# Kernel tuning notes

Measured on AMD Instinct MI355X. Metric: run time of the kernel, lower is better.

Reference implementation:

```python
import math
import jax, jax.numpy as jnp
import numpy as np

# dims (from init_kwargs / forward signature)
B, N, K = 8, 1024, 8            # batch, nodes, num_neighbors
NC, TED, TEC = 64, 128, 64      # num_channels, time_embedding_dim, time_embedding_channels
C = NC + TEC                    # model dim = 128
H, Dh = 8, 16                   # heads, dim_head
HD = H * Dh
L = 4                           # num_layers
RH = 32                         # radial-net hidden width
NPATH = 10                      # radial scalars: k00,k10,k01,k11a,k11b,v00,v10,v01,v11a,v11b


def _g(k, shape, fan_in):
    return jax.random.normal(k, shape, dtype=jnp.float32) / np.sqrt(float(fan_in))


def setup_inputs() -> dict:
    key = jax.random.key(0)
    ks = jax.random.split(key, 16)
    return dict(
        x=jax.random.normal(ks[0], (B, N, 3), dtype=jnp.float32),
        y=jax.random.normal(ks[1], (B, N, 3), dtype=jnp.float32),
        t=jax.random.uniform(ks[2], (B,), dtype=jnp.float32) * 1000.0,
        Wt1=_g(ks[3], (TED, TED), TED), bt1=jnp.zeros((TED,), jnp.float32),
        Wt2=_g(ks[4], (TED, TEC), TED), bt2=jnp.zeros((TEC,), jnp.float32),
        Win0=_g(ks[5], (TEC + 3, C), TEC + 3), bin0=jnp.zeros((C,), jnp.float32),
        Win1=_g(ks[6], (1, C), 1),
        Wqkv=_g(ks[7], (L, 12, C, HD), C),           # q0,q1,k00,k10,k01,k11a,k11b,v00,v10,v01,v11a,v11b
        Wr1=_g(ks[8], (L, 1, RH), 1), br1=jnp.zeros((L, RH), jnp.float32),
        Wr2=_g(ks[9], (L, RH, H * NPATH), RH), br2=jnp.zeros((L, H * NPATH), jnp.float32),
        Wo=_g(ks[10], (L, 2, HD, C), HD), bo=jnp.zeros((L, 2, C), jnp.float32),
        Wout=_g(ks[11], (3, C), C), bout=jnp.zeros((3,), jnp.float32),
    )


def _forward(x, y, t, Wt1, bt1, Wt2, bt2, Win0, bin0, Win1, Wqkv,
             Wr1, br1, Wr2, br2, Wo, bo, Wout, bout):
    b, n = x.shape[0], x.shape[1]
    # sinusoidal time embedding + time MLP
    half = TED // 2
    freqs = jnp.exp(-math.log(10000.0) * jnp.arange(half, dtype=x.dtype) / half)
    emb = t[:, None] * freqs
    temb = jnp.concatenate([jnp.sin(emb), jnp.cos(emb)], axis=-1)          # [B,TED]
    temb = jax.nn.silu(temb @ Wt1 + bt1) @ Wt2 + bt2                        # [B,TEC]

    # degree-0 input = [time_embed | coords], degree-1 input = coords (1 channel)
    deg0 = jnp.concatenate([jnp.broadcast_to(temb[:, None, :], (b, n, TEC)), x], axis=-1)
    f0 = deg0 @ Win0 + bin0                                                 # [B,N,C]
    f1 = jnp.einsum('bnv,c->bncv', x, Win1[0])                              # [B,N,C,3]

    # k-nearest-neighbor graph on coordinates (shared across layers)
    d2 = jnp.sum((x[:, :, None, :] - x[:, None, :, :]) ** 2, axis=-1)       # [B,N,N]
    d2 = d2 + jnp.eye(n, dtype=x.dtype) * 1e9                               # exclude self
    _, idx = jax.lax.top_k(-d2, K)                                          # [B,N,K]
    gather = lambda f: jax.vmap(lambda a, i: a[i])(f, idx)                  # [B,N,...] -> [B,N,K,...]
    rel = gather(x) - x[:, :, None, :]                                      # [B,N,K,3]
    r = jnp.sqrt(jnp.sum(rel ** 2, axis=-1, keepdims=True) + 1e-8)          # [B,N,K,1]
    rhat = rel / r

    inv_scale = 1.0 / float(np.sqrt(2 * Dh))
    for l in range(L):
        Wl = Wqkv[l].reshape(12, C, H, Dh)
        q0 = jnp.einsum('bnc,chd->bnhd', f0, Wl[0])
        q1 = jnp.einsum('bncv,chd->bnhdv', f1, Wl[1])
        f0j, f1j = gather(f0), gather(f1)                                   # [B,N,K,C], [B,N,K,C,3]
        # radial network -> per-head, per-path scalars
        Rn = (jax.nn.silu(r @ Wr1[l] + br1[l]) @ Wr2[l] + br2[l]).reshape(b, n, K, H, NPATH)
        # equivariant tensor-product paths (degrees 0/1, spherical harmonics Y0,Y1,Y2)
        dot1 = jnp.einsum('bnkcv,bnkv->bnkc', f1j, rhat)                    # 1->0 path
        sym = 3.0 * dot1[..., None] * rhat[:, :, :, None, :] - f1j          # Y2 (traceless sym) 1->1 path
        p0 = lambda f, w: jnp.einsum('bnkc,chd->bnkhd', f, w)
        p1 = lambda f, w: jnp.einsum('bnkcv,chd->bnkhdv', f, w)
        rh = rhat[:, :, :, None, None, :]
        k0 = p0(f0j, Wl[2]) * Rn[..., 0:1] + p0(dot1, Wl[3]) * Rn[..., 1:2]
        k1 = (p0(f0j, Wl[4])[..., None] * rh * Rn[..., 2][..., None, None]
              + p1(f1j, Wl[5]) * Rn[..., 3][..., None, None]
              + p1(sym, Wl[6]) * Rn[..., 4][..., None, None])
        v0 = p0(f0j, Wl[7]) * Rn[..., 5:6] + p0(dot1, Wl[8]) * Rn[..., 6:7]
        v1 = (p0(f0j, Wl[9])[..., None] * rh * Rn[..., 7][..., None, None]
              + p1(f1j, Wl[10]) * Rn[..., 8][..., None, None]
              + p1(sym, Wl[11]) * Rn[..., 9][..., None, None])
        logits = (jnp.einsum('bnhd,bnkhd->bnhk', q0, k0)
                  + jnp.einsum('bnhdv,bnkhdv->bnhk', q1, k1)) * inv_scale
        attn = jax.nn.softmax(logits, axis=-1)
        o0 = jnp.einsum('bnhk,bnkhd->bnhd', attn, v0).reshape(b, n, HD)
        o1 = jnp.einsum('bnhk,bnkhdv->bnhdv', attn, v1).reshape(b, n, HD, 3)
        f0 = f0 + o0 @ Wo[l, 0] + bo[l, 0]
        f1 = f1 + jnp.einsum('bnev,ec->bncv', o1, Wo[l, 1]) + bo[l, 1][None, None, :, None]

    # output layer Linear(dim, 3) applied as per-component channel mixing on the type-1 output
    return jnp.einsum('bncv,vc->bnv', f1, Wout) + bout                      # [B,N,3]


def reference(x, y, t, Wt1, bt1, Wt2, bt2, Win0, bin0, Win1, Wqkv,
              Wr1, br1, Wr2, br2, Wo, bo, Wout, bout):
    return _forward(x, y, t, Wt1, bt1, Wt2, bt2, Win0, bin0, Win1, Wqkv,
                    Wr1, br1, Wr2, br2, Wo, bo, Wout, bout)
```

## Files before the change

kernel.cpp:

```cpp
#include <hip/hip_runtime.h>
#include <math.h>

#define NBATCH 8
#define NPTS   1024
#define KNN    8
#define CC     128
#define HD_    128
#define TED_   128
#define TEC_   64
#define RH     32
#define NL     4

typedef _Float16 half8 __attribute__((ext_vector_type(8)));
typedef _Float16 h2v  __attribute__((ext_vector_type(2)));
typedef float f32x4 __attribute__((ext_vector_type(4)));

__global__ __launch_bounds__(128) void k_temb(
    const float* __restrict__ t, const float* __restrict__ Wt1,
    const float* __restrict__ bt1, const float* __restrict__ Wt2,
    const float* __restrict__ bt2, const float* __restrict__ Win0,
    const float* __restrict__ bin0, float* __restrict__ pre0)
{
  int b = blockIdx.x;
  int tid = threadIdx.x;
  __shared__ float e128[TED_];
  __shared__ float h1[TED_];
  __shared__ float te[TEC_];
  float tv = t[b];
  if (tid < 64) {
    float fr = expf((-9.210340371976184f * (float)tid) * 0.015625f);
    float em = tv * fr;
    e128[tid]      = sinf(em);
    e128[tid + 64] = cosf(em);
  }
  __syncthreads();
  {
    float acc = bt1[tid];
    for (int i = 0; i < TED_; ++i) acc += e128[i] * Wt1[i * TED_ + tid];
    h1[tid] = acc / (1.0f + expf(-acc));
  }
  __syncthreads();
  if (tid < TEC_) {
    float acc = bt2[tid];
    for (int j = 0; j < TED_; ++j) acc += h1[j] * Wt2[j * TEC_ + tid];
    te[tid] = acc;
  }
  __syncthreads();
  {
    float acc = bin0[tid];
    for (int i = 0; i < TEC_; ++i) acc += te[i] * Win0[i * CC + tid];
    pre0[b * CC + tid] = acc;
  }
}

__global__ __launch_bounds__(256) void k_init(
    const float* __restrict__ x, const float* __restrict__ Win0,
    const float* __restrict__ Win1, const float* __restrict__ pre0,
    float* __restrict__ f0, float* __restrict__ f1,
    _Float16* __restrict__ f0h, _Float16* __restrict__ f1h)
{
  int node = blockIdx.x * 2 + (threadIdx.x >> 7);
  int c = threadIdx.x & 127;
  int b = node >> 10;
  float x0 = x[node * 3 + 0], x1 = x[node * 3 + 1], x2 = x[node * 3 + 2];
  float acc = pre0[b * CC + c]
            + x0 * Win0[(TEC_ + 0) * CC + c]
            + x1 * Win0[(TEC_ + 1) * CC + c]
            + x2 * Win0[(TEC_ + 2) * CC + c];
  f0[(size_t)node * CC + c] = acc;
  f0h[(size_t)node * CC + c] = (_Float16)acc;
  float w1 = Win1[c];
  float v0 = x0 * w1, v1 = x1 * w1, v2 = x2 * w1;
  f1[((size_t)node * 3 + 0) * CC + c] = v0;
  f1[((size_t)node * 3 + 1) * CC + c] = v1;
  f1[((size_t)node * 3 + 2) * CC + c] = v2;
  f1h[((size_t)node * 3 + 0) * CC + c] = (_Float16)v0;
  f1h[((size_t)node * 3 + 1) * CC + c] = (_Float16)v1;
  f1h[((size_t)node * 3 + 2) * CC + c] = (_Float16)v2;
}

__global__ __launch_bounds__(256) void k_knn(
    const float* __restrict__ x, int* __restrict__ idx,
    float* __restrict__ rhat, float* __restrict__ rl)
{
  const int b    = blockIdx.x >> 5;
  const int tile = blockIdx.x & 31;
  const int tid  = threadIdx.x;
  const int qg   = tid >> 3;
  const int sub  = tid & 7;

  __shared__ float xs[NPTS * 3];
  __shared__ unsigned long long keys[32][64];

  for (int i = tid; i < NPTS * 3; i += 256) xs[i] = x[(size_t)b * NPTS * 3 + i];
  __syncthreads();

  const int n = tile * 32 + qg;
  const float qx = xs[n * 3 + 0], qy = xs[n * 3 + 1], qz = xs[n * 3 + 2];

  unsigned long long bd[KNN];
  #pragma unroll
  for (int k = 0; k < KNN; ++k) bd[k] = ~0ull;

  const int j0 = sub * 128;
  for (int j = j0; j < j0 + 128; ++j) {
    float dx = qx - xs[j * 3 + 0];
    float dy = qy - xs[j * 3 + 1];
    float dz = qz - xs[j * 3 + 2];
    float s = __fadd_rn(__fadd_rn(__fmul_rn(dx, dx), __fmul_rn(dy, dy)),
                        __fmul_rn(dz, dz));
    if (j == n) s = 1.0e9f;
    unsigned long long key =
        ((unsigned long long)__float_as_uint(s) << 32) | (unsigned int)j;
    if (key < bd[KNN - 1]) {
      bd[KNN - 1] = key;
      #pragma unroll
      for (int q = KNN - 1; q > 0; --q) {
        if (bd[q] < bd[q - 1]) {
          unsigned long long tmp = bd[q]; bd[q] = bd[q - 1]; bd[q - 1] = tmp;
        }
      }
    }
  }
  #pragma unroll
  for (int k = 0; k < KNN; ++k) keys[qg][sub * KNN + k] = bd[k];
  __syncthreads();

  if (sub == 0) {
    unsigned long long m[KNN];
    #pragma unroll
    for (int k = 0; k < KNN; ++k) m[k] = ~0ull;
    for (int i = 0; i < 64; ++i) {
      unsigned long long key = keys[qg][i];
      if (key < m[KNN - 1]) {
        m[KNN - 1] = key;
        #pragma unroll
        for (int q = KNN - 1; q > 0; --q) {
          if (m[q] < m[q - 1]) {
            unsigned long long tmp = m[q]; m[q] = m[q - 1]; m[q - 1] = tmp;
          }
        }
      }
    }
    size_t base = ((size_t)b * NPTS + n) * KNN;
    #pragma unroll
    for (int k = 0; k < KNN; ++k) {
      int j = (int)(m[k] & 0xffffffffu);
      idx[base + k] = j;
      float rx = xs[j * 3 + 0] - qx;
      float ry = xs[j * 3 + 1] - qy;
      float rz = xs[j * 3 + 2] - qz;
      float rr2 = rx * rx + ry * ry + rz * rz + 1e-8f;
      float r = sqrtf(rr2);
      rl[base + k] = r;
      rhat[(base + k) * 3 + 0] = rx / r;
      rhat[(base + k) * 3 + 1] = ry / r;
      rhat[(base + k) * 3 + 2] = rz / r;
    }
  }
}

__global__ __launch_bounds__(256) void k_wconv(
    const float* __restrict__ Wqkv, const float* __restrict__ Wo,
    _Float16* __restrict__ Whq, _Float16* __restrict__ Who)
{
  __shared__ _Float16 T[128][136];
  int m = blockIdx.x;
  const float* src; _Float16* dst;
  if (m < 48) { src = Wqkv + (size_t)m * 16384; dst = Whq + (size_t)m * 16384; }
  else { src = Wo + (size_t)(m - 48) * 16384; dst = Who + (size_t)(m - 48) * 16384; }
  int tid = threadIdx.x;
  for (int i = tid; i < 16384; i += 256) {
    int k = i >> 7, n = i & 127;
    T[n][k] = (_Float16)src[i];
  }
  __syncthreads();
  for (int i = tid; i < 16384; i += 256) {
    int n = i >> 7, k = i & 127;
    dst[i] = T[n][k];
  }
}

#define MFMA_BODY(A_, ROWBASE_, WT_)                                          \
  const int tid  = threadIdx.x;                                               \
  const int lane = tid & 63;                                                  \
  const int w    = tid >> 6;                                                  \
  const int r15  = lane & 15;                                                 \
  const int g    = lane >> 4;                                                 \
  half8 bf[2][4];                                                             \
  _Pragma("unroll")                                                           \
  for (int ntl = 0; ntl < 2; ++ntl) {                                         \
    int n = (w * 2 + ntl) * 16 + r15;                                         \
    const _Float16* wp = (WT_) + (size_t)n * 128 + g * 8;                     \
    _Pragma("unroll")                                                         \
    for (int ks = 0; ks < 4; ++ks)                                            \
      bf[ntl][ks] = *(const half8*)(wp + ks * 32);                            \
  }                                                                           \
  {                                                                           \
    int r = tid >> 1;                                                         \
    const _Float16* src = (A_) + (size_t)((ROWBASE_) + r) * 128;              \
    int c0 = (tid & 1) * 8;                                                   \
    _Pragma("unroll")                                                         \
    for (int q = 0; q < 8; ++q) {                                             \
      int c = c0 + q;                                                         \
      *(uint4*)&As[r][c * 8] = *(const uint4*)(src + c * 8);                  \
    }                                                                         \
  }                                                                           \
  __syncthreads();                                                            \
  f32x4 acc[8][2] = {};                                                       \
  _Pragma("unroll")                                                           \
  for (int ks = 0; ks < 4; ++ks) {                                            \
    half8 a[8];                                                               \
    _Pragma("unroll")                                                         \
    for (int mt = 0; mt < 8; ++mt)                                            \
      a[mt] = *(const half8*)&As[mt * 16 + r15][ks * 32 + g * 8];             \
    _Pragma("unroll")                                                         \
    for (int mt = 0; mt < 8; ++mt) {                                          \
      acc[mt][0] = __builtin_amdgcn_mfma_f32_16x16x32_f16(a[mt], bf[0][ks], acc[mt][0], 0, 0, 0); \
      acc[mt][1] = __builtin_amdgcn_mfma_f32_16x16x32_f16(a[mt], bf[1][ks], acc[mt][1], 0, 0, 0); \
    }                                                                         \
  }

__global__ __launch_bounds__(256) void k_proj_mfma(
    const _Float16* __restrict__ f0h, const _Float16* __restrict__ f1h,
    const _Float16* __restrict__ Wh, _Float16* __restrict__ P0,
    _Float16* __restrict__ P1, int nb0)
{
  __shared__ _Float16 As[128][136];
  int z = blockIdx.x;
  const _Float16* A; const _Float16* Wt; _Float16* P; int ldP, colBase, rowBase;
  if (z < nb0 * 5) {
    const int map0[5] = {0, 2, 4, 7, 9};
    int m = z / nb0, rb = z - m * nb0;
    A = f0h; rowBase = rb * 128;
    Wt = Wh + (size_t)map0[m] * 16384;
    P = P0; ldP = 640; colBase = m * 128;
  } else {
    z -= nb0 * 5;
    int nb1 = nb0 * 3;
    const int map1[7] = {1, 3, 5, 6, 8, 10, 11};
    int m = z / nb1, rb = z - m * nb1;
    A = f1h; rowBase = rb * 128;
    Wt = Wh + (size_t)map1[m] * 16384;
    P = P1; ldP = 896; colBase = m * 128;
  }
  MFMA_BODY(A, rowBase, Wt)
  #pragma unroll
  for (int mt = 0; mt < 8; ++mt) {
    #pragma unroll
    for (int ntl = 0; ntl < 2; ++ntl) {
      int col = colBase + (w * 2 + ntl) * 16 + r15;
      #pragma unroll
      for (int i = 0; i < 4; ++i) {
        int r = rowBase + mt * 16 + g * 4 + i;
        P[(size_t)r * ldP + col] = (_Float16)acc[mt][ntl][i];
      }
    }
  }
}

__global__ __launch_bounds__(256) void k_wo_mfma(
    const _Float16* __restrict__ o0h, const _Float16* __restrict__ o1h,
    const _Float16* __restrict__ Who_l, const float* __restrict__ bo_l,
    float* __restrict__ f0, float* __restrict__ f1,
    _Float16* __restrict__ f0h, _Float16* __restrict__ f1h, int nb0)
{
  __shared__ _Float16 As[128][136];
  int z = blockIdx.x;
  const _Float16* A; const _Float16* Wt; const float* bias;
  float* F; _Float16* FH; int rowBase;
  if (z < nb0) {
    A = o0h; Wt = Who_l; bias = bo_l; F = f0; FH = f0h; rowBase = z * 128;
  } else {
    z -= nb0;
    A = o1h; Wt = Who_l + 16384; bias = bo_l + CC; F = f1; FH = f1h; rowBase = z * 128;
  }
  MFMA_BODY(A, rowBase, Wt)
  #pragma unroll
  for (int mt = 0; mt < 8; ++mt) {
    #pragma unroll
    for (int ntl = 0; ntl < 2; ++ntl) {
      int col = (w * 2 + ntl) * 16 + r15;
      float bv = bias[col];
      #pragma unroll
      for (int i = 0; i < 4; ++i) {
        int r = rowBase + mt * 16 + g * 4 + i;
        size_t p = (size_t)r * 128 + col;
        float val = F[p] + acc[mt][ntl][i] + bv;
        F[p] = val;
        FH[p] = (_Float16)val;
      }
    }
  }
}

__global__ __launch_bounds__(256) void k_attn(
    const _Float16* __restrict__ P0, const _Float16* __restrict__ P1,
    const int* __restrict__ idx, const float* __restrict__ rhat,
    const float* __restrict__ rl,
    const float* __restrict__ Wr1, const float* __restrict__ br1,
    const float* __restrict__ Wr2, const float* __restrict__ br2,
    _Float16* __restrict__ o0h, _Float16* __restrict__ o1h,
    int nodeBase, int layer, int nbg)
{
  const int t = threadIdx.x;
  const int wv = t >> 6;
  const int lane = t & 63;
  const int z = blockIdx.x;
  const int bb = z % nbg;
  const int nodeLocal = bb * NPTS + (z / nbg) * 4 + wv;
  const int node = nodeBase + nodeLocal;
  const int batchRow = bb * NPTS;

  __shared__ float rn_s[4][KNN][80];
  __shared__ float hid_s[4][KNN][RH];
  __shared__ float rh_s[4][KNN][3];
  __shared__ float rl_s[4][KNN];

  if (lane < KNN * 3) rh_s[wv][lane / 3][lane % 3] = rhat[(size_t)node * KNN * 3 + lane];
  if (lane >= 32 && lane < 32 + KNN) rl_s[wv][lane - 32] = rl[(size_t)node * KNN + (lane - 32)];
  __syncthreads();

  const float* wr1 = Wr1 + layer * RH;
  const float* wb1 = br1 + layer * RH;
  #pragma unroll
  for (int u = 0; u < 4; ++u) {
    int f = u * 64 + lane;
    int k = f >> 5, i = f & 31;
    float zv = rl_s[wv][k] * wr1[i] + wb1[i];
    hid_s[wv][k][i] = zv / (1.0f + expf(-zv));
  }
  __syncthreads();
  const float* wr2 = Wr2 + layer * RH * 80;
  const float* wb2 = br2 + layer * 80;
  #pragma unroll
  for (int u = 0; u < 10; ++u) {
    int f = u * 64 + lane;
    int k = f / 80, col = f - k * 80;
    float acc = wb2[col];
    #pragma unroll
    for (int i = 0; i < RH; ++i) acc += hid_s[wv][k][i] * wr2[i * 80 + col];
    rn_s[wv][k][col] = acc;
  }
  __syncthreads();

  const int c0 = lane * 2;
  const int h = lane >> 3;
  const _Float16* p0n = P0 + (size_t)nodeLocal * 640 + c0;
  const _Float16* p1n = P1 + (size_t)nodeLocal * 2688 + c0;
  h2v q0v  = *(const h2v*)(p0n);
  h2v q1xv = *(const h2v*)(p1n);
  h2v q1yv = *(const h2v*)(p1n + 896);
  h2v q1zv = *(const h2v*)(p1n + 1792);

  const float inv_scale = 0.17677669529663687f;
  const int* idxp = idx + (size_t)node * KNN;

  float m = -3.0e38f, ssum = 0.0f;
  float a0[2] = {}, ax[2] = {}, ay[2] = {}, az[2] = {};

  for (int k = 0; k < KNN; ++k) {
    int jl = batchRow + idxp[k];
    const _Float16* g0 = P0 + (size_t)jl * 640 + c0;
    const _Float16* g1 = P1 + (size_t)jl * 2688 + c0;
    float rx = rh_s[wv][k][0], ry = rh_s[wv][k][1], rz = rh_s[wv][k][2];

    h2v G02 = *(const h2v*)(g0 + 128), G04 = *(const h2v*)(g0 + 256);
    h2v G07 = *(const h2v*)(g0 + 384), G09 = *(const h2v*)(g0 + 512);
    h2v G13x = *(const h2v*)(g1 + 128),  G13y = *(const h2v*)(g1 + 896 + 128),  G13z = *(const h2v*)(g1 + 1792 + 128);
    h2v G15x = *(const h2v*)(g1 + 256),  G15y = *(const h2v*)(g1 + 896 + 256),  G15z = *(const h2v*)(g1 + 1792 + 256);
    h2v G16x = *(const h2v*)(g1 + 384),  G16y = *(const h2v*)(g1 + 896 + 384),  G16z = *(const h2v*)(g1 + 1792 + 384);
    h2v G18x = *(const h2v*)(g1 + 512),  G18y = *(const h2v*)(g1 + 896 + 512),  G18z = *(const h2v*)(g1 + 1792 + 512);
    h2v G1Ax = *(const h2v*)(g1 + 640),  G1Ay = *(const h2v*)(g1 + 896 + 640),  G1Az = *(const h2v*)(g1 + 1792 + 640);
    h2v G1Bx = *(const h2v*)(g1 + 768),  G1By = *(const h2v*)(g1 + 896 + 768),  G1Bz = *(const h2v*)(g1 + 1792 + 768);

    const float* rnh = &rn_s[wv][k][h * 10];
    float r0 = rnh[0], r1 = rnh[1], r2 = rnh[2], r3 = rnh[3], r4 = rnh[4];
    float r5 = rnh[5], r6 = rnh[6], r7 = rnh[7], r8 = rnh[8], r9 = rnh[9];

    float pl = 0.0f;
    float v0c[2], vxc[2], vyc[2], vzc[2];
    #pragma unroll
    for (int ci = 0; ci < 2; ++ci) {
      float g02 = (float)G02[ci], g04 = (float)G04[ci];
      float g07 = (float)G07[ci], g09 = (float)G09[ci];
      float g13x = (float)G13x[ci], g13y = (float)G13y[ci], g13z = (float)G13z[ci];
      float g15x = (float)G15x[ci], g15y = (float)G15y[ci], g15z = (float)G15z[ci];
      float g16x = (float)G16x[ci], g16y = (float)G16y[ci], g16z = (float)G16z[ci];
      float g18x = (float)G18x[ci], g18y = (float)G18y[ci], g18z = (float)G18z[ci];
      float g1ax = (float)G1Ax[ci], g1ay = (float)G1Ay[ci], g1az = (float)G1Az[ci];
      float g1bx = (float)G1Bx[ci], g1by = (float)G1By[ci], g1bz = (float)G1Bz[ci];

      float DP3 = g13x * rx + g13y * ry + g13z * rz;
      float DP6 = g16x * rx + g16y * ry + g16z * rz;
      float DP8 = g18x * rx + g18y * ry + g18z * rz;
      float DPB = g1bx * rx + g1by * ry + g1bz * rz;

      float k0  = g02 * r0 + DP3 * r1;
      float k1x = g04 * rx * r2 + g15x * r3 + (3.0f * rx * DP6 - g16x) * r4;
      float k1y = g04 * ry * r2 + g15y * r3 + (3.0f * ry * DP6 - g16y) * r4;
      float k1z = g04 * rz * r2 + g15z * r3 + (3.0f * rz * DP6 - g16z) * r4;
      v0c[ci] = g07 * r5 + DP8 * r6;
      vxc[ci] = g09 * rx * r7 + g1ax * r8 + (3.0f * rx * DPB - g1bx) * r9;
      vyc[ci] = g09 * ry * r7 + g1ay * r8 + (3.0f * ry * DPB - g1by) * r9;
      vzc[ci] = g09 * rz * r7 + g1az * r8 + (3.0f * rz * DPB - g1bz) * r9;

      pl += (float)((ci == 0) ? q0v[0] : q0v[1]) * k0
          + (float)((ci == 0) ? q1xv[0] : q1xv[1]) * k1x
          + (float)((ci == 0) ? q1yv[0] : q1yv[1]) * k1y
          + (float)((ci == 0) ? q1zv[0] : q1zv[1]) * k1z;
    }
    pl += __shfl_xor(pl, 1, 8);
    pl += __shfl_xor(pl, 2, 8);
    pl += __shfl_xor(pl, 4, 8);
    pl *= inv_scale;

    float mnew = fmaxf(m, pl);
    float scale = expf(m - mnew);
    float wgt = expf(pl - mnew);
    ssum = ssum * scale + wgt;
    #pragma unroll
    for (int ci = 0; ci < 2; ++ci) {
      a0[ci] = a0[ci] * scale + wgt * v0c[ci];
      ax[ci] = ax[ci] * scale + wgt * vxc[ci];
      ay[ci] = ay[ci] * scale + wgt * vyc[ci];
      az[ci] = az[ci] * scale + wgt * vzc[ci];
    }
    m = mnew;
  }

  float invs = 1.0f / ssum;
  h2v o;
  o[0] = (_Float16)(a0[0] * invs); o[1] = (_Float16)(a0[1] * invs);
  *(h2v*)(o0h + (size_t)nodeLocal * 128 + c0) = o;
  o[0] = (_Float16)(ax[0] * invs); o[1] = (_Float16)(ax[1] * invs);
  *(h2v*)(o1h + ((size_t)nodeLocal * 3 + 0) * 128 + c0) = o;
  o[0] = (_Float16)(ay[0] * invs); o[1] = (_Float16)(ay[1] * invs);
  *(h2v*)(o1h + ((size_t)nodeLocal * 3 + 1) * 128 + c0) = o;
  o[0] = (_Float16)(az[0] * invs); o[1] = (_Float16)(az[1] * invs);
  *(h2v*)(o1h + ((size_t)nodeLocal * 3 + 2) * 128 + c0) = o;
}

__global__ __launch_bounds__(256) void k_out(
    const float* __restrict__ f1, const float* __restrict__ Wout,
    const float* __restrict__ bout, float* __restrict__ out)
{
  int i = blockIdx.x * 256 + threadIdx.x;
  int v = i % 3;
  const float* row = f1 + (size_t)i * CC;
  const float* w = Wout + v * CC;
  float acc = 0.0f;
  #pragma unroll
  for (int c = 0; c < CC; c += 4) {
    float4 fv = *(const float4*)&row[c];
    float4 wv = *(const float4*)&w[c];
    acc += fv.x * wv.x + fv.y * wv.y + fv.z * wv.z + fv.w * wv.w;
  }
  out[i] = acc + bout[v];
}

extern "C" void kernel_launch(void* const* d_in, const int* in_sizes, int n_in,
                              void* d_out, int out_size, void* d_ws, size_t ws_size,
                              hipStream_t stream) {
  const float* x    = (const float*)d_in[0];
  const float* t    = (const float*)d_in[2];
  const float* Wt1  = (const float*)d_in[3];
  const float* bt1  = (const float*)d_in[4];
  const float* Wt2  = (const float*)d_in[5];
  const float* bt2  = (const float*)d_in[6];
  const float* Win0 = (const float*)d_in[7];
  const float* bin0 = (const float*)d_in[8];
  const float* Win1 = (const float*)d_in[9];
  const float* Wqkv = (const float*)d_in[10];
  const float* Wr1  = (const float*)d_in[11];
  const float* br1  = (const float*)d_in[12];
  const float* Wr2  = (const float*)d_in[13];
  const float* br2  = (const float*)d_in[14];
  const float* Wo   = (const float*)d_in[15];
  const float* bo   = (const float*)d_in[16];
  const float* Wout = (const float*)d_in[17];
  const float* bout = (const float*)d_in[18];
  float* out = (float*)d_out;

  char* wsb = (char*)d_ws;
  size_t off = 0;
  auto alloc = [&](size_t bytes) -> void* {
    void* p = wsb + off;
    off = (off + bytes + 255) & ~(size_t)255;
    return p;
  };
  const int totalNodes = NBATCH * NPTS;
  float* pre0 = (float*)alloc((size_t)NBATCH * CC * 4);
  float* f0   = (float*)alloc((size_t)totalNodes * CC * 4);
  float* f1   = (float*)alloc((size_t)totalNodes * 3 * CC * 4);
  _Float16* f0h = (_Float16*)alloc((size_t)totalNodes * CC * 2);
  _Float16* f1h = (_Float16*)alloc((size_t)totalNodes * 3 * CC * 2);
  _Float16* Whq = (_Float16*)alloc((size_t)NL * 12 * CC * HD_ * 2);
  _Float16* Who = (_Float16*)alloc((size_t)NL * 2 * CC * HD_ * 2);
  int*   idx  = (int*)alloc((size_t)totalNodes * KNN * 4);
  float* rhat = (float*)alloc((size_t)totalNodes * KNN * 3 * 4);
  float* rl   = (float*)alloc((size_t)totalNodes * KNN * 4);
  size_t fixedBytes = off;
  size_t perBatch = (size_t)NPTS * ((640 + 2688) * 2 + (128 + 384) * 2);
  int nbg = 8;
  while (nbg > 1 && fixedBytes + (size_t)nbg * perBatch + 8192 > ws_size) nbg >>= 1;
  _Float16* P0  = (_Float16*)alloc((size_t)nbg * NPTS * 640 * 2);
  _Float16* P1  = (_Float16*)alloc((size_t)nbg * NPTS * 2688 * 2);
  _Float16* o0h = (_Float16*)alloc((size_t)nbg * NPTS * 128 * 2);
  _Float16* o1h = (_Float16*)alloc((size_t)nbg * NPTS * 384 * 2);

  k_temb<<<NBATCH, 128, 0, stream>>>(t, Wt1, bt1, Wt2, bt2, Win0, bin0, pre0);
  k_init<<<totalNodes / 2, 256, 0, stream>>>(x, Win0, Win1, pre0, f0, f1, f0h, f1h);
  k_knn<<<NBATCH * 32, 256, 0, stream>>>(x, idx, rhat, rl);
  k_wconv<<<56, 256, 0, stream>>>(Wqkv, Wo, Whq, Who);

  for (int g = 0; g < NBATCH / nbg; ++g) {
    int nodeBase = g * nbg * NPTS;
    int nodes = nbg * NPTS;
    int nb0 = nodes / 128;
    for (int l = 0; l < NL; ++l) {
      k_proj_mfma<<<nb0 * 26, 256, 0, stream>>>(
          f0h + (size_t)nodeBase * CC, f1h + (size_t)nodeBase * 3 * CC,
          Whq + (size_t)l * 12 * CC * HD_, P0, P1, nb0);
      k_attn<<<nodes / 4, 256, 0, stream>>>(
          P0, P1, idx, rhat, rl, Wr1, br1, Wr2, br2, o0h, o1h, nodeBase, l, nbg);
      k_wo_mfma<<<nb0 * 4, 256, 0, stream>>>(
          o0h, o1h, Who + (size_t)l * 2 * CC * HD_, bo + (size_t)(l * 2) * CC,
          f0 + (size_t)nodeBase * CC, f1 + (size_t)nodeBase * 3 * CC,
          f0h + (size_t)nodeBase * CC, f1h + (size_t)nodeBase * 3 * CC, nb0);
    }
  }
  k_out<<<(totalNodes * 3) / 256, 256, 0, stream>>>(f1, Wout, bout, out);
}
```

Measured before the change: 469.6 us.

## Widen attention lanes to 4 channels and merge kNN partial lists via shuffles

The attention kernel now maps one node per 32-lane half-wave with 4 channels per lane, using 8-byte fp16 loads, a 2-step shuffle reduction, and half as many blocks; the radial MLP is computed cooperatively for 8 nodes per block. The kNN kernel switches to SoA shared coordinates with staggered iteration, and replaces the shared-memory serial merge by a shuffle-based 8-way min extraction, so each of the 8 sub-lanes writes one neighbor. This aims to cut gather instruction count, serialized merge work and shared-memory traffic, at the cost of more registers per lane in attention.

```diff
diff --git a/kernel.cpp b/kernel.cpp
--- a/kernel.cpp
+++ b/kernel.cpp
@@ -12,8 +12,12 @@
 #define NL     4
 
 typedef _Float16 half8 __attribute__((ext_vector_type(8)));
-typedef _Float16 h2v  __attribute__((ext_vector_type(2)));
+typedef _Float16 h4v  __attribute__((ext_vector_type(4)));
 typedef float f32x4 __attribute__((ext_vector_type(4)));
+
+__device__ __forceinline__ unsigned long long shflxor_u64(unsigned long long v, int m) {
+  return (unsigned long long)__shfl_xor((long long)v, m, 8);
+}
 
 __global__ __launch_bounds__(128) void k_temb(
     const float* __restrict__ t, const float* __restrict__ Wt1,
@@ -89,24 +93,28 @@
   const int qg   = tid >> 3;
   const int sub  = tid & 7;
 
-  __shared__ float xs[NPTS * 3];
-  __shared__ unsigned long long keys[32][64];
-
-  for (int i = tid; i < NPTS * 3; i += 256) xs[i] = x[(size_t)b * NPTS * 3 + i];
+  __shared__ float xsx[NPTS], xsy[NPTS], xsz[NPTS];
+
+  for (int i = tid; i < NPTS; i += 256) {
+    const float* xp = x + ((size_t)b * NPTS + i) * 3;
+    xsx[i] = xp[0]; xsy[i] = xp[1]; xsz[i] = xp[2];
+  }
   __syncthreads();
 
   const int n = tile * 32 + qg;
-  const float qx = xs[n * 3 + 0], qy = xs[n * 3 + 1], qz = xs[n * 3 + 2];
+  const float qx = xsx[n], qy = xsy[n], qz = xsz[n];
 
   unsigned long long bd[KNN];
   #pragma unroll
   for (int k = 0; k < KNN; ++k) bd[k] = ~0ull;
 
   const int j0 = sub * 128;
-  for (int j = j0; j < j0 + 128; ++j) {
-    float dx = qx - xs[j * 3 + 0];
-    float dy = qy - xs[j * 3 + 1];
-    float dz = qz - xs[j * 3 + 2];
+  const int ph = sub * 4;
+  for (int it = 0; it < 128; ++it) {
+    int j = j0 + ((it + ph) & 127);
+    float dx = qx - xsx[j];
+    float dy = qy - xsy[j];
+    float dz = qz - xsz[j];
     float s = __fadd_rn(__fadd_rn(__fmul_rn(dx, dx), __fmul_rn(dy, dy)),
                         __fmul_rn(dz, dz));
     if (j == n) s = 1.0e9f;
@@ -122,42 +130,38 @@
       }
     }
   }
-  #pragma unroll
-  for (int k = 0; k < KNN; ++k) keys[qg][sub * KNN + k] = bd[k];
-  __syncthreads();
-
-  if (sub == 0) {
-    unsigned long long m[KNN];
-    #pragma unroll
-    for (int k = 0; k < KNN; ++k) m[k] = ~0ull;
-    for (int i = 0; i < 64; ++i) {
-      unsigned long long key = keys[qg][i];
-      if (key < m[KNN - 1]) {
-        m[KNN - 1] = key;
-        #pragma unroll
-        for (int q = KNN - 1; q > 0; --q) {
-          if (m[q] < m[q - 1]) {
-            unsigned long long tmp = m[q]; m[q] = m[q - 1]; m[q - 1] = tmp;
-          }
-        }
-      }
-    }
-    size_t base = ((size_t)b * NPTS + n) * KNN;
-    #pragma unroll
-    for (int k = 0; k < KNN; ++k) {
-      int j = (int)(m[k] & 0xffffffffu);
-      idx[base + k] = j;
-      float rx = xs[j * 3 + 0] - qx;
-      float ry = xs[j * 3 + 1] - qy;
-      float rz = xs[j * 3 + 2] - qz;
-      float rr2 = rx * rx + ry * ry + rz * rz + 1e-8f;
-      float r = sqrtf(rr2);
-      rl[base + k] = r;
-      rhat[(base + k) * 3 + 0] = rx / r;
-      rhat[(base + k) * 3 + 1] = ry / r;
-      rhat[(base + k) * 3 + 2] = rz / r;
-    }
-  }
+
+  unsigned long long res[KNN];
+  #pragma unroll
+  for (int r = 0; r < KNN; ++r) {
+    unsigned long long m = bd[0];
+    unsigned long long o;
+    o = shflxor_u64(m, 1); m = (o < m) ? o : m;
+    o = shflxor_u64(m, 2); m = (o < m) ? o : m;
+    o = shflxor_u64(m, 4); m = (o < m) ? o : m;
+    if (bd[0] == m) {
+      #pragma unroll
+      for (int q = 0; q < KNN - 1; ++q) bd[q] = bd[q + 1];
+      bd[KNN - 1] = ~0ull;
+    }
+    res[r] = m;
+  }
+
+  unsigned long long key = res[0];
+  #pragma unroll
+  for (int r = 1; r < KNN; ++r) if (sub == r) key = res[r];
+  int j = (int)(key & 0xffffffffu);
+  size_t base = ((size_t)b * NPTS + n) * KNN + sub;
+  idx[base] = j;
+  float rx = xsx[j] - qx;
+  float ry = xsy[j] - qy;
+  float rz = xsz[j] - qz;
+  float rr2 = rx * rx + ry * ry + rz * rz + 1e-8f;
+  float r = sqrtf(rr2);
+  rl[base] = r;
+  rhat[base * 3 + 0] = rx / r;
+  rhat[base * 3 + 1] = ry / r;
+  rhat[base * 3 + 2] = rz / r;
 }
 
 __global__ __launch_bounds__(256) void k_wconv(
@@ -304,84 +308,99 @@
     int nodeBase, int layer, int nbg)
 {
   const int t = threadIdx.x;
-  const int wv = t >> 6;
-  const int lane = t & 63;
+  const int wv = t >> 5;
+  const int lane = t & 31;
   const int z = blockIdx.x;
   const int bb = z % nbg;
-  const int nodeLocal = bb * NPTS + (z / nbg) * 4 + wv;
+  const int qbase = (z / nbg) * 8;
+  const int nodeLocal = bb * NPTS + qbase + wv;
   const int node = nodeBase + nodeLocal;
   const int batchRow = bb * NPTS;
 
-  __shared__ float rn_s[4][KNN][80];
-  __shared__ float hid_s[4][KNN][RH];
-  __shared__ float rh_s[4][KNN][3];
-  __shared__ float rl_s[4][KNN];
-
-  if (lane < KNN * 3) rh_s[wv][lane / 3][lane % 3] = rhat[(size_t)node * KNN * 3 + lane];
-  if (lane >= 32 && lane < 32 + KNN) rl_s[wv][lane - 32] = rl[(size_t)node * KNN + (lane - 32)];
+  __shared__ float rn_s[8][KNN][80];
+  __shared__ float hid_s[8][KNN][RH];
+  __shared__ float rh_s[8][KNN][3];
+  __shared__ float rl_s[8][KNN];
+
+  {
+    int f = t;
+    if (f < 192) {
+      int nd = f / 24, e = f % 24;
+      rh_s[nd][e / 3][e % 3] =
+          rhat[((size_t)(nodeBase + bb * NPTS + qbase + nd)) * KNN * 3 + e];
+    } else {
+      int f2 = f - 192;
+      int nd = f2 >> 3, k = f2 & 7;
+      rl_s[nd][k] = rl[((size_t)(nodeBase + bb * NPTS + qbase + nd)) * KNN + k];
+    }
+  }
   __syncthreads();
 
   const float* wr1 = Wr1 + layer * RH;
   const float* wb1 = br1 + layer * RH;
   #pragma unroll
-  for (int u = 0; u < 4; ++u) {
-    int f = u * 64 + lane;
-    int k = f >> 5, i = f & 31;
-    float zv = rl_s[wv][k] * wr1[i] + wb1[i];
-    hid_s[wv][k][i] = zv / (1.0f + expf(-zv));
+  for (int u = 0; u < 8; ++u) {
+    int f = u * 256 + t;
+    int nd = f >> 8, k = (f >> 5) & 7, i = f & 31;
+    float zv = rl_s[nd][k] * wr1[i] + wb1[i];
+    hid_s[nd][k][i] = zv / (1.0f + expf(-zv));
   }
   __syncthreads();
   const float* wr2 = Wr2 + layer * RH * 80;
   const float* wb2 = br2 + layer * 80;
   #pragma unroll
-  for (int u = 0; u < 10; ++u) {
-    int f = u * 64 + lane;
-    int k = f / 80, col = f - k * 80;
+  for (int u = 0; u < 20; ++u) {
+    int f = u * 256 + t;
+    int nd = f / 640, rem = f - nd * 640;
+    int k = rem / 80, col = rem - k * 80;
     float acc = wb2[col];
     #pragma unroll
-    for (int i = 0; i < RH; ++i) acc += hid_s[wv][k][i] * wr2[i * 80 + col];
-    rn_s[wv][k][col] = acc;
-  }
-  __syncthreads();
-
-  const int c0 = lane * 2;
-  const int h = lane >> 3;
+    for (int i = 0; i < RH; ++i) acc += hid_s[nd][k][i] * wr2[i * 80 + col];
+    rn_s[nd][k][col] = acc;
+  }
+  __syncthreads();
+
+  const int c0 = lane * 4;
+  const int h = lane >> 2;
   const _Float16* p0n = P0 + (size_t)nodeLocal * 640 + c0;
   const _Float16* p1n = P1 + (size_t)nodeLocal * 2688 + c0;
-  h2v q0v  = *(const h2v*)(p0n);
-  h2v q1xv = *(const h2v*)(p1n);
-  h2v q1yv = *(const h2v*)(p1n + 896);
-  h2v q1zv = *(const h2v*)(p1n + 1792);
+  h4v q0v  = *(const h4v*)(p0n);
+  h4v q1xv = *(const h4v*)(p1n);
+  h4v q1yv = *(const h4v*)(p1n + 896);
+  h4v q1zv = *(const h4v*)(p1n + 1792);
 
   const float inv_scale = 0.17677669529663687f;
   const int* idxp = idx + (size_t)node * KNN;
+  int jls[KNN];
+  #pragma unroll
+  for (int k = 0; k < KNN; ++k) jls[k] = batchRow + idxp[k];
 
   float m = -3.0e38f, ssum = 0.0f;
-  float a0[2] = {}, ax[2] = {}, ay[2] = {}, az[2] = {};
+  float a0[4] = {}, ax[4] = {}, ay[4] = {}, az[4] = {};
 
   for (int k = 0; k < KNN; ++k) {
-    int jl = batchRow + idxp[k];
+    int jl = jls[k];
     const _Float16* g0 = P0 + (size_t)jl * 640 + c0;
     const _Float16* g1 = P1 + (size_t)jl * 2688 + c0;
     float rx = rh_s[wv][k][0], ry = rh_s[wv][k][1], rz = rh_s[wv][k][2];
 
-    h2v G02 = *(const h2v*)(g0 + 128), G04 = *(const h2v*)(g0 + 256);
-    h2v G07 = *(const h2v*)(g0 + 384), G09 = *(const h2v*)(g0 + 512);
-    h2v G13x = *(const h2v*)(g1 + 128),  G13y = *(const h2v*)(g1 + 896 + 128),  G13z = *(const h2v*)(g1 + 1792 + 128);
-    h2v G15x = *(const h2v*)(g1 + 256),  G15y = *(const h2v*)(g1 + 896 + 256),  G15z = *(const h2v*)(g1 + 1792 + 256);
-    h2v G16x = *(const h2v*)(g1 + 384),  G16y = *(const h2v*)(g1 + 896 + 384),  G16z = *(const h2v*)(g1 + 1792 + 384);
-    h2v G18x = *(const h2v*)(g1 + 512),  G18y = *(const h2v*)(g1 + 896 + 512),  G18z = *(const h2v*)(g1 + 1792 + 512);
-    h2v G1Ax = *(const h2v*)(g1 + 640),  G1Ay = *(const h2v*)(g1 + 896 + 640),  G1Az = *(const h2v*)(g1 + 1792 + 640);
-    h2v G1Bx = *(const h2v*)(g1 + 768),  G1By = *(const h2v*)(g1 + 896 + 768),  G1Bz = *(const h2v*)(g1 + 1792 + 768);
+    h4v G02 = *(const h4v*)(g0 + 128), G04 = *(const h4v*)(g0 + 256);
+    h4v G07 = *(const h4v*)(g0 + 384), G09 = *(const h4v*)(g0 + 512);
+    h4v G13x = *(const h4v*)(g1 + 128),  G13y = *(const h4v*)(g1 + 896 + 128),  G13z = *(const h4v*)(g1 + 1792 + 128);
+    h4v G15x = *(const h4v*)(g1 + 256),  G15y = *(const h4v*)(g1 + 896 + 256),  G15z = *(const h4v*)(g1 + 1792 + 256);
+    h4v G16x = *(const h4v*)(g1 + 384),  G16y = *(const h4v*)(g1 + 896 + 384),  G16z = *(const h4v*)(g1 + 1792 + 384);
+    h4v G18x = *(const h4v*)(g1 + 512),  G18y = *(const h4v*)(g1 + 896 + 512),  G18z = *(const h4v*)(g1 + 1792 + 512);
+    h4v G1Ax = *(const h4v*)(g1 + 640),  G1Ay = *(const h4v*)(g1 + 896 + 640),  G1Az = *(const h4v*)(g1 + 1792 + 640);
+    h4v G1Bx = *(const h4v*)(g1 + 768),  G1By = *(const h4v*)(g1 + 896 + 768),  G1Bz = *(const h4v*)(g1 + 1792 + 768);
 
     const float* rnh = &rn_s[wv][k][h * 10];
     float r0 = rnh[0], r1 = rnh[1], r2 = rnh[2], r3 = rnh[3], r4 = rnh[4];
     float r5 = rnh[5], r6 = rnh[6], r7 = rnh[7], r8 = rnh[8], r9 = rnh[9];
 
     float pl = 0.0f;
-    float v0c[2], vxc[2], vyc[2], vzc[2];
+    float v0c[4], vxc[4], vyc[4], vzc[4];
     #pragma unroll
-    for (int ci = 0; ci < 2; ++ci) {
+    for (int ci = 0; ci < 4; ++ci) {
       float g02 = (float)G02[ci], g04 = (float)G04[ci];
       float g07 = (float)G07[ci], g09 = (float)G09[ci];
       float g13x = (float)G13x[ci], g13y = (float)G13y[ci], g13z = (float)G13z[ci];
@@ -405,14 +424,11 @@
       vyc[ci] = g09 * ry * r7 + g1ay * r8 + (3.0f * ry * DPB - g1by) * r9;
       vzc[ci] = g09 * rz * r7 + g1az * r8 + (3.0f * rz * DPB - g1bz) * r9;
 
-      pl += (float)((ci == 0) ? q0v[0] : q0v[1]) * k0
-          + (float)((ci == 0) ? q1xv[0] : q1xv[1]) * k1x
-          + (float)((ci == 0) ? q1yv[0] : q1yv[1]) * k1y
-          + (float)((ci == 0) ? q1zv[0] : q1zv[1]) * k1z;
-    }
-    pl += __shfl_xor(pl, 1, 8);
-    pl += __shfl_xor(pl, 2, 8);
-    pl += __shfl_xor(pl, 4, 8);
+      pl += (float)q0v[ci] * k0 + (float)q1xv[ci] * k1x
+          + (float)q1yv[ci] * k1y + (float)q1zv[ci] * k1z;
+    }
+    pl += __shfl_xor(pl, 1, 4);
+    pl += __shfl_xor(pl, 2, 4);
     pl *= inv_scale;
 
     float mnew = fmaxf(m, pl);
@@ -420,7 +436,7 @@
     float wgt = expf(pl - mnew);
     ssum = ssum * scale + wgt;
     #pragma unroll
-    for (int ci = 0; ci < 2; ++ci) {
+    for (int ci = 0; ci < 4; ++ci) {
       a0[ci] = a0[ci] * scale + wgt * v0c[ci];
       ax[ci] = ax[ci] * scale + wgt * vxc[ci];
       ay[ci] = ay[ci] * scale + wgt * vyc[ci];
@@ -430,15 +446,19 @@
   }
 
   float invs = 1.0f / ssum;
-  h2v o;
-  o[0] = (_Float16)(a0[0] * invs); o[1] = (_Float16)(a0[1] * invs);
-  *(h2v*)(o0h + (size_t)nodeLocal * 128 + c0) = o;
-  o[0] = (_Float16)(ax[0] * invs); o[1] = (_Float16)(ax[1] * invs);
-  *(h2v*)(o1h + ((size_t)nodeLocal * 3 + 0) * 128 + c0) = o;
-  o[0] = (_Float16)(ay[0] * invs); o[1] = (_Float16)(ay[1] * invs);
-  *(h2v*)(o1h + ((size_t)nodeLocal * 3 + 1) * 128 + c0) = o;
-  o[0] = (_Float16)(az[0] * invs); o[1] = (_Float16)(az[1] * invs);
-  *(h2v*)(o1h + ((size_t)nodeLocal * 3 + 2) * 128 + c0) = o;
+  h4v o;
+  #pragma unroll
+  for (int ci = 0; ci < 4; ++ci) o[ci] = (_Float16)(a0[ci] * invs);
+  *(h4v*)(o0h + (size_t)nodeLocal * 128 + c0) = o;
+  #pragma unroll
+  for (int ci = 0; ci < 4; ++ci) o[ci] = (_Float16)(ax[ci] * invs);
+  *(h4v*)(o1h + ((size_t)nodeLocal * 3 + 0) * 128 + c0) = o;
+  #pragma unroll
+  for (int ci = 0; ci < 4; ++ci) o[ci] = (_Float16)(ay[ci] * invs);
+  *(h4v*)(o1h + ((size_t)nodeLocal * 3 + 1) * 128 + c0) = o;
+  #pragma unroll
+  for (int ci = 0; ci < 4; ++ci) o[ci] = (_Float16)(az[ci] * invs);
+  *(h4v*)(o1h + ((size_t)nodeLocal * 3 + 2) * 128 + c0) = o;
 }
 
 __global__ __launch_bounds__(256) void k_out(
@@ -522,7 +542,7 @@
       k_proj_mfma<<<nb0 * 26, 256, 0, stream>>>(
           f0h + (size_t)nodeBase * CC, f1h + (size_t)nodeBase * 3 * CC,
           Whq + (size_t)l * 12 * CC * HD_, P0, P1, nb0);
-      k_attn<<<nodes / 4, 256, 0, stream>>>(
+      k_attn<<<nodes / 8, 256, 0, stream>>>(
           P0, P1, idx, rhat, rl, Wr1, br1, Wr2, br2, o0h, o1h, nodeBase, l, nbg);
       k_wo_mfma<<<nb0 * 4, 256, 0, stream>>>(
           o0h, o1h, Who + (size_t)l * 2 * CC * HD_, bo + (size_t)(l * 2) * CC,
```

After: 463.9 us. No clear change (-1.2%).
